# Kernel tuning notes

Hardware: AMD Instinct MI355X
Metric: run time of the kernel (lower is better)

Reference implementation:

```python
import jax, jax.numpy as jnp
import numpy as np

D = 8       # latent dim d
NE = 4      # n_emb
NS = 3      # n_outer stages
NI = 5      # n_inner iterations per stage
EPS = 1e-5  # LayerNorm eps
TAU = 1.0   # route_tau (default), max(1.0, 1e-3) = 1.0


def _ln(x, g, b):
    m = x.mean(-1, keepdims=True)
    v = ((x - m) ** 2).mean(-1, keepdims=True)
    return (x - m) / jnp.sqrt(v + EPS) * g + b


def _inner(E, u, Bm, Wp, bp, W1, b1, W2, b2):
    # E: [B, NE, D], u: [B, D]
    Bsz = E.shape[0]
    # bilinear interaction: outer product e_i u^T + B_i, for all i at once
    M = E[:, :, :, None] * u[:, None, None, :] + Bm[None]      # [B, NE, D, D]
    H = M.reshape(Bsz, NE, D * D) @ Wp.T + bp                  # W_proj: [B, NE, D]
    # softmax routing: s_i = softmax(route(h_i)/tau) over experts
    lg = jax.nn.relu(H @ W1.T + b1) @ W2.T + b2                # [B, NE, NE]
    s = jax.nn.softmax(lg / TAU, axis=-1)
    mix = jnp.einsum('bne,bed->bnd', s, H)                     # per-i mixture of H
    return E + mix


def setup_inputs() -> dict:
    B = 131072
    key = jax.random.key(0)
    ks = jax.random.split(key, 32)
    f32 = jnp.float32
    inp = {
        'cl':     jax.random.normal(ks[0], (B,), f32),
        'cd':     jax.random.normal(ks[1], (B,), f32),
        're_log': jax.random.normal(ks[2], (B,), f32),
        'mach':   jax.random.normal(ks[3], (B,), f32),
        'alpha':  jax.random.normal(ks[4], (B,), f32),
        'u':      jax.random.normal(ks[5], (B, D), f32),
        'We':    jax.random.normal(ks[6], (NE, D, 2), f32) * 0.5,
        'be':    jnp.zeros((NE, D), f32),
        # per-stage InnerBlockAblated params (stacked over NS stages)
        'Bmat':  jax.random.normal(ks[7], (NS, NE, D, D), f32) * 0.05,
        'Wproj': jax.random.normal(ks[8], (NS, D, D * D), f32) * 0.1,
        'bproj': jnp.zeros((NS, D), f32),
        'Wr1':   jax.random.normal(ks[9], (NS, D, D), f32) * 0.3,
        'br1':   jnp.zeros((NS, D), f32),
        'Wr2':   jax.random.normal(ks[10], (NS, NE, D), f32) * 0.3,
        'br2':   jnp.zeros((NS, NE), f32),
        # post-stage LayerNorm
        'ln_g':  jnp.ones((D,), f32),
        'ln_b':  jnp.zeros((D,), f32),
        # final mixing over embeddings: Linear(n_emb*d, n_emb)
        'Wout':  jax.random.normal(ks[11], (NE, NE * D), f32) * 0.1,
        'bout':  jnp.zeros((NE,), f32),
        # final LayerNorm
        'fg':    jnp.ones((D,), f32),
        'fb':    jnp.zeros((D,), f32),
        # heads: head_cst Linear(d, 18), head_cl Linear(d, 1)
        'Wcst':  jax.random.normal(ks[12], (18, D), f32) * 0.2,
        'bcst':  jnp.zeros((18,), f32),
        'Wcl':   jax.random.normal(ks[13], (1, D), f32) * 0.2,
        'bcl':   jnp.zeros((1,), f32),
    }
    return inp


def reference(cl, cd, re_log, mach, alpha, u, We, be, Bmat, Wproj, bproj,
              Wr1, br1, Wr2, br2, ln_g, ln_b, Wout, bout, fg, fb,
              Wcst, bcst, Wcl, bcl):
    # _stack_pairs: [B, 4, 2]
    pairs = jnp.stack([
        jnp.stack([cl, alpha], -1),
        jnp.stack([cd, alpha], -1),
        jnp.stack([re_log, alpha], -1),
        jnp.stack([mach, alpha], -1),
    ], axis=1)
    # embed: per-embedding Linear(2, d) + Tanh  -> E: [B, NE, D]
    E = jnp.tanh(jnp.einsum('bne,nde->bnd', pairs, We) + be[None])
    # outer stages: n_inner inner blocks each, then post-stage LayerNorm
    for s_idx in range(NS):
        for _ in range(NI):
            E = _inner(E, u, Bmat[s_idx], Wproj[s_idx], bproj[s_idx],
                       Wr1[s_idx], br1[s_idx], Wr2[s_idx], br2[s_idx])
        E = _ln(E, ln_g, ln_b)
    # final softmax mixing over embeddings (w_out_logits)
    Bsz = E.shape[0]
    w = jax.nn.softmax(E.reshape(Bsz, NE * D) @ Wout.T + bout, axis=-1)  # [B, NE]
    z = _ln(jnp.einsum('bn,bnd->bd', w, E), fg, fb)                       # [B, D]
    # heads, concatenated: [B, 18 + 1]
    return jnp.concatenate([z @ Wcst.T + bcst, z @ Wcl.T + bcl], axis=-1)
```

## Files before the change

kernel.cpp:

```cpp
#include <hip/hip_runtime.h>

#define D 8
#define NE 4
#define NS 3
#define NI 5
#define LN_EPS 1e-5f

#define OFF_W1 0
#define OFF_W2 192
#define OFF_B1 288
#define OFF_B2 312
#define OFF_C  324
#define OFF_LN 420
#define OFF_WP 436
#define WLDS_SIZE 1972

__global__ void precompute_C_kernel(const float* __restrict__ Bmat,
                                    const float* __restrict__ Wproj,
                                    const float* __restrict__ bproj,
                                    float* __restrict__ C) {
    int idx = threadIdx.x;
    if (idx >= NS * NE * D) return;
    int s = idx / (NE * D);
    int rem = idx % (NE * D);
    int n = rem / D;
    int d = rem % D;
    const float* bm = Bmat + ((size_t)s * NE + n) * 64;
    const float* wp = Wproj + ((size_t)s * D + d) * 64;
    float acc = bproj[s * D + d];
    #pragma unroll
    for (int k = 0; k < 64; ++k) acc += bm[k] * wp[k];
    C[idx] = acc;
}

__device__ __forceinline__ float fast_tanh(float x) {
    float e = __expf(2.f * x);
    return 1.f - 2.f * __builtin_amdgcn_rcpf(e + 1.f);
}

__device__ __forceinline__ float4 ld4(const float* p) {
    return *reinterpret_cast<const float4*>(p);
}

__global__ __launch_bounds__(256, 2) void whisp_kernel(
    const float* __restrict__ cl, const float* __restrict__ cd,
    const float* __restrict__ re_log, const float* __restrict__ mach,
    const float* __restrict__ alpha, const float* __restrict__ u,
    const float* __restrict__ We, const float* __restrict__ be,
    const float* __restrict__ Wproj,
    const float* __restrict__ Wr1, const float* __restrict__ br1,
    const float* __restrict__ Wr2, const float* __restrict__ br2,
    const float* __restrict__ ln_g, const float* __restrict__ ln_b,
    const float* __restrict__ Wout, const float* __restrict__ bout,
    const float* __restrict__ fg, const float* __restrict__ fb,
    const float* __restrict__ Wcst, const float* __restrict__ bcst,
    const float* __restrict__ Wcl, const float* __restrict__ bcl,
    const float* __restrict__ Cpre,
    float* __restrict__ out, int B)
{
    __shared__ __align__(16) float wlds[WLDS_SIZE];
    __shared__ __align__(16) float4 tbuf[16 * 256];

    const int tid = threadIdx.x;
    const int row0 = blockIdx.x * 256 + tid;
    const bool active = (row0 < B);
    const int row = active ? row0 : (B - 1);

    for (int i = tid; i < 192;  i += 256) wlds[OFF_W1 + i] = Wr1[i];
    for (int i = tid; i < 96;   i += 256) wlds[OFF_W2 + i] = Wr2[i];
    for (int i = tid; i < 24;   i += 256) wlds[OFF_B1 + i] = br1[i];
    for (int i = tid; i < 12;   i += 256) wlds[OFF_B2 + i] = br2[i];
    for (int i = tid; i < 96;   i += 256) wlds[OFF_C + i]  = Cpre[i];
    for (int i = tid; i < 8;    i += 256) { wlds[OFF_LN + i] = ln_g[i]; wlds[OFF_LN + 8 + i] = ln_b[i]; }
    for (int i = tid; i < 1536; i += 256) wlds[OFF_WP + i] = Wproj[i];

    float uu[D];
    {
        const float4* up = reinterpret_cast<const float4*>(u + (size_t)row * D);
        float4 u0 = up[0], u1 = up[1];
        uu[0]=u0.x; uu[1]=u0.y; uu[2]=u0.z; uu[3]=u0.w;
        uu[4]=u1.x; uu[5]=u1.y; uu[6]=u1.z; uu[7]=u1.w;
    }
    float xs[NE] = { cl[row], cd[row], re_log[row], mach[row] };
    float al = alpha[row];

    float E[NE][D];
    #pragma unroll
    for (int n = 0; n < NE; ++n) {
        #pragma unroll
        for (int d = 0; d < D; ++d) {
            float pre = We[n * 16 + d * 2 + 0] * xs[n]
                      + We[n * 16 + d * 2 + 1] * al
                      + be[n * D + d];
            E[n][d] = fast_tanh(pre);
        }
    }

    __syncthreads();

    int zero = 0;

    #pragma unroll 1
    for (int s = 0; s < NS; ++s) {
        {
            const float* Wp = wlds + OFF_WP + s * 512;
            #pragma unroll
            for (int d = 0; d < D; ++d) {
                float tv[D];
                #pragma unroll
                for (int i = 0; i < D; ++i) {
                    float4 wa = ld4(Wp + d * 64 + i * 8);
                    float4 wb = ld4(Wp + d * 64 + i * 8 + 4);
                    float a0 = uu[0] * wa.x, a1 = uu[1] * wa.y;
                    a0 = fmaf(uu[2], wa.z, a0); a1 = fmaf(uu[3], wa.w, a1);
                    a0 = fmaf(uu[4], wb.x, a0); a1 = fmaf(uu[5], wb.y, a1);
                    a0 = fmaf(uu[6], wb.z, a0); a1 = fmaf(uu[7], wb.w, a1);
                    tv[i] = a0 + a1;
                }
                tbuf[(2 * d) * 256 + tid]     = make_float4(tv[0], tv[1], tv[2], tv[3]);
                tbuf[(2 * d + 1) * 256 + tid] = make_float4(tv[4], tv[5], tv[6], tv[7]);
            }
        }

        float b1a[8], b2a[4];
        {
            float4 q0 = ld4(wlds + OFF_B1 + s * 8);
            float4 q1 = ld4(wlds + OFF_B1 + s * 8 + 4);
            b1a[0]=q0.x; b1a[1]=q0.y; b1a[2]=q0.z; b1a[3]=q0.w;
            b1a[4]=q1.x; b1a[5]=q1.y; b1a[6]=q1.z; b1a[7]=q1.w;
            float4 q2 = ld4(wlds + OFF_B2 + s * 4);
            b2a[0]=q2.x; b2a[1]=q2.y; b2a[2]=q2.z; b2a[3]=q2.w;
        }

        #pragma unroll 1
        for (int it = 0; it < NI; ++it) {
            asm volatile("" : "+v"(zero));
            const float*  W1z = wlds + OFF_W1 + s * 64 + zero;
            const float*  W2z = wlds + OFF_W2 + s * 32 + zero;
            const float*  Cz  = wlds + OFF_C  + s * 32 + zero;
            const float4* tz  = tbuf + tid + zero;

            float H[NE][D];
            #pragma unroll
            for (int n = 0; n < NE; ++n) {
                float4 c0 = ld4(Cz + n * 8);
                float4 c1 = ld4(Cz + n * 8 + 4);
                H[n][0]=c0.x; H[n][1]=c0.y; H[n][2]=c0.z; H[n][3]=c0.w;
                H[n][4]=c1.x; H[n][5]=c1.y; H[n][6]=c1.z; H[n][7]=c1.w;
            }
            #pragma unroll
            for (int d = 0; d < D; ++d) {
                float4 ta = tz[(2 * d) * 256];
                float4 tb = tz[(2 * d + 1) * 256];
                #pragma unroll
                for (int n = 0; n < NE; ++n) {
                    float a0 = fmaf(E[n][0], ta.x, H[n][d]);
                    float a1 = E[n][1] * ta.y;
                    a0 = fmaf(E[n][2], ta.z, a0);
                    a1 = fmaf(E[n][3], ta.w, a1);
                    a0 = fmaf(E[n][4], tb.x, a0);
                    a1 = fmaf(E[n][5], tb.y, a1);
                    a0 = fmaf(E[n][6], tb.z, a0);
                    a1 = fmaf(E[n][7], tb.w, a1);
                    H[n][d] = a0 + a1;
                }
            }

            float sm[NE][NE];
            #pragma unroll
            for (int n = 0; n < NE; ++n) {
                float r[D];
                #pragma unroll
                for (int d = 0; d < D; ++d) {
                    float4 wa = ld4(W1z + d * 8);
                    float4 wb = ld4(W1z + d * 8 + 4);
                    float a0 = fmaf(H[n][0], wa.x, b1a[d]);
                    float a1 = H[n][1] * wa.y;
                    a0 = fmaf(H[n][2], wa.z, a0);
                    a1 = fmaf(H[n][3], wa.w, a1);
                    a0 = fmaf(H[n][4], wb.x, a0);
                    a1 = fmaf(H[n][5], wb.y, a1);
                    a0 = fmaf(H[n][6], wb.z, a0);
                    a1 = fmaf(H[n][7], wb.w, a1);
                    r[d] = fmaxf(a0 + a1, 0.f);
                }
                float lg[NE];
                #pragma unroll
                for (int e = 0; e < NE; ++e) {
                    float4 wa = ld4(W2z + e * 8);
                    float4 wb = ld4(W2z + e * 8 + 4);
                    float a0 = fmaf(r[0], wa.x, b2a[e]);
                    float a1 = r[1] * wa.y;
                    a0 = fmaf(r[2], wa.z, a0);
                    a1 = fmaf(r[3], wa.w, a1);
                    a0 = fmaf(r[4], wb.x, a0);
                    a1 = fmaf(r[5], wb.y, a1);
                    a0 = fmaf(r[6], wb.z, a0);
                    a1 = fmaf(r[7], wb.w, a1);
                    lg[e] = a0 + a1;
                }
                float mx = fmaxf(fmaxf(lg[0], lg[1]), fmaxf(lg[2], lg[3]));
                float e0 = __expf(lg[0] - mx), e1 = __expf(lg[1] - mx);
                float e2 = __expf(lg[2] - mx), e3 = __expf(lg[3] - mx);
                float inv = __builtin_amdgcn_rcpf((e0 + e1) + (e2 + e3));
                sm[n][0] = e0 * inv; sm[n][1] = e1 * inv;
                sm[n][2] = e2 * inv; sm[n][3] = e3 * inv;
            }

            #pragma unroll
            for (int n = 0; n < NE; ++n) {
                #pragma unroll
                for (int d = 0; d < D; ++d) {
                    float a0 = fmaf(sm[n][0], H[0][d], E[n][d]);
                    float a1 = sm[n][1] * H[1][d];
                    a0 = fmaf(sm[n][2], H[2][d], a0);
                    a1 = fmaf(sm[n][3], H[3][d], a1);
                    E[n][d] = a0 + a1;
                }
            }
        }

        float lngv[8], lnbv[8];
        {
            float4 g0 = ld4(wlds + OFF_LN),     g1 = ld4(wlds + OFF_LN + 4);
            float4 b0 = ld4(wlds + OFF_LN + 8), b1 = ld4(wlds + OFF_LN + 12);
            lngv[0]=g0.x; lngv[1]=g0.y; lngv[2]=g0.z; lngv[3]=g0.w;
            lngv[4]=g1.x; lngv[5]=g1.y; lngv[6]=g1.z; lngv[7]=g1.w;
            lnbv[0]=b0.x; lnbv[1]=b0.y; lnbv[2]=b0.z; lnbv[3]=b0.w;
            lnbv[4]=b1.x; lnbv[5]=b1.y; lnbv[6]=b1.z; lnbv[7]=b1.w;
        }
        #pragma unroll
        for (int n = 0; n < NE; ++n) {
            float m = 0.f;
            #pragma unroll
            for (int d = 0; d < D; ++d) m += E[n][d];
            m *= (1.f / D);
            float v = 0.f;
            #pragma unroll
            for (int d = 0; d < D; ++d) { float c = E[n][d] - m; v = fmaf(c, c, v); }
            v *= (1.f / D);
            float inv = __builtin_amdgcn_rsqf(v + LN_EPS);
            #pragma unroll
            for (int d = 0; d < D; ++d)
                E[n][d] = (E[n][d] - m) * inv * lngv[d] + lnbv[d];
        }
    }

    float lgf[NE];
    #pragma unroll
    for (int e = 0; e < NE; ++e) {
        float a0 = bout[e], a1 = 0.f;
        #pragma unroll
        for (int n = 0; n < NE; ++n) {
            #pragma unroll
            for (int d = 0; d < D; d += 2) {
                a0 = fmaf(E[n][d],     Wout[e * 32 + n * D + d],     a0);
                a1 = fmaf(E[n][d + 1], Wout[e * 32 + n * D + d + 1], a1);
            }
        }
        lgf[e] = a0 + a1;
    }
    float mx = fmaxf(fmaxf(lgf[0], lgf[1]), fmaxf(lgf[2], lgf[3]));
    float w0 = __expf(lgf[0] - mx), w1 = __expf(lgf[1] - mx);
    float w2 = __expf(lgf[2] - mx), w3 = __expf(lgf[3] - mx);
    float winv = __builtin_amdgcn_rcpf((w0 + w1) + (w2 + w3));
    w0 *= winv; w1 *= winv; w2 *= winv; w3 *= winv;

    float z[D];
    #pragma unroll
    for (int d = 0; d < D; ++d) {
        float a0 = w0 * E[0][d];
        float a1 = w1 * E[1][d];
        a0 = fmaf(w2, E[2][d], a0);
        a1 = fmaf(w3, E[3][d], a1);
        z[d] = a0 + a1;
    }
    float zm = 0.f;
    #pragma unroll
    for (int d = 0; d < D; ++d) zm += z[d];
    zm *= (1.f / D);
    float zv = 0.f;
    #pragma unroll
    for (int d = 0; d < D; ++d) { float c = z[d] - zm; zv = fmaf(c, c, zv); }
    zv *= (1.f / D);
    float zinv = __builtin_amdgcn_rsqf(zv + LN_EPS);
    #pragma unroll
    for (int d = 0; d < D; ++d)
        z[d] = (z[d] - zm) * zinv * fg[d] + fb[d];

    float zout[19];
    #pragma unroll
    for (int k = 0; k < 18; ++k) {
        float a0 = bcst[k], a1 = 0.f;
        #pragma unroll
        for (int d = 0; d < D; d += 2) {
            a0 = fmaf(z[d],     Wcst[k * D + d],     a0);
            a1 = fmaf(z[d + 1], Wcst[k * D + d + 1], a1);
        }
        zout[k] = a0 + a1;
    }
    {
        float a0 = bcl[0], a1 = 0.f;
        #pragma unroll
        for (int d = 0; d < D; d += 2) {
            a0 = fmaf(z[d],     Wcl[d],     a0);
            a1 = fmaf(z[d + 1], Wcl[d + 1], a1);
        }
        zout[18] = a0 + a1;
    }

    __syncthreads();
    float* souts = reinterpret_cast<float*>(tbuf);
    if (active) {
        #pragma unroll
        for (int k = 0; k < 19; ++k) souts[tid * 19 + k] = zout[k];
    }
    __syncthreads();

    const int base = blockIdx.x * 256;
    int nrows = B - base;
    if (nrows > 256) nrows = 256;
    if (nrows > 0) {
        const int cnt = nrows * 19;
        for (int i = tid; i < cnt; i += 256)
            out[(size_t)base * 19 + i] = souts[i];
    }
}

extern "C" void kernel_launch(void* const* d_in, const int* in_sizes, int n_in,
                              void* d_out, int out_size, void* d_ws, size_t ws_size,
                              hipStream_t stream) {
    const float* cl     = (const float*)d_in[0];
    const float* cd     = (const float*)d_in[1];
    const float* re_log = (const float*)d_in[2];
    const float* mach   = (const float*)d_in[3];
    const float* alpha  = (const float*)d_in[4];
    const float* u      = (const float*)d_in[5];
    const float* We     = (const float*)d_in[6];
    const float* be     = (const float*)d_in[7];
    const float* Bmat   = (const float*)d_in[8];
    const float* Wproj  = (const float*)d_in[9];
    const float* bproj  = (const float*)d_in[10];
    const float* Wr1    = (const float*)d_in[11];
    const float* br1    = (const float*)d_in[12];
    const float* Wr2    = (const float*)d_in[13];
    const float* br2    = (const float*)d_in[14];
    const float* ln_g   = (const float*)d_in[15];
    const float* ln_b   = (const float*)d_in[16];
    const float* Wout   = (const float*)d_in[17];
    const float* bout   = (const float*)d_in[18];
    const float* fg     = (const float*)d_in[19];
    const float* fb     = (const float*)d_in[20];
    const float* Wcst   = (const float*)d_in[21];
    const float* bcst   = (const float*)d_in[22];
    const float* Wcl    = (const float*)d_in[23];
    const float* bcl    = (const float*)d_in[24];

    float* Cpre = (float*)d_ws;
    const int B = in_sizes[0];

    hipLaunchKernelGGL(precompute_C_kernel, dim3(1), dim3(128), 0, stream,
                       Bmat, Wproj, bproj, Cpre);

    const int blocks = (B + 255) / 256;
    hipLaunchKernelGGL(whisp_kernel, dim3(blocks), dim3(256), 0, stream,
                       cl, cd, re_log, mach, alpha, u, We, be, Wproj,
                       Wr1, br1, Wr2, br2, ln_g, ln_b, Wout, bout, fg, fb,
                       Wcst, bcst, Wcl, bcl, Cpre, (float*)d_out, B);
}
```

Baseline: 72.29 us.

## Vectorize inner block with packed float2 FMAs across embedding pairs

Reorganizes the per-row state so pairs of embeddings are held in float2 vectors, letting the compiler emit packed FP32 FMA instructions (v_pk_fma_f32) for the bilinear projection, routing MLP, softmax mixing and LayerNorm. The C precompute and W2 weights are relaid out in shared memory to match the paired layout, and the router's two layers are fused so logits accumulate directly per hidden unit. This aims to halve VALU instruction count in the compute-bound inner loop, at the cost of broadcast operand shuffles and possible register pressure changes.

```diff
diff --git a/kernel.cpp b/kernel.cpp
--- a/kernel.cpp
+++ b/kernel.cpp
@@ -6,14 +6,20 @@
 #define NI 5
 #define LN_EPS 1e-5f
 
-#define OFF_W1 0
-#define OFF_W2 192
-#define OFF_B1 288
-#define OFF_B2 312
-#define OFF_C  324
-#define OFF_LN 420
-#define OFF_WP 436
+#define OFF_W1  0
+#define OFF_W2T 192
+#define OFF_B1  288
+#define OFF_B2  312
+#define OFF_C   324
+#define OFF_LN  420
+#define OFF_WP  436
 #define WLDS_SIZE 1972
+
+typedef float f2 __attribute__((ext_vector_type(2)));
+
+__device__ __forceinline__ f2 fma2(f2 a, f2 b, f2 c) { return __builtin_elementwise_fma(a, b, c); }
+__device__ __forceinline__ f2 max2(f2 a, f2 b) { return __builtin_elementwise_max(a, b); }
+__device__ __forceinline__ f2 bc(float s) { return (f2){s, s}; }
 
 __global__ void precompute_C_kernel(const float* __restrict__ Bmat,
                                     const float* __restrict__ Wproj,
@@ -30,7 +36,7 @@
     float acc = bproj[s * D + d];
     #pragma unroll
     for (int k = 0; k < 64; ++k) acc += bm[k] * wp[k];
-    C[idx] = acc;
+    C[s * 32 + ((n >> 1) * 8 + d) * 2 + (n & 1)] = acc;
 }
 
 __device__ __forceinline__ float fast_tanh(float x) {
@@ -67,7 +73,10 @@
     const int row = active ? row0 : (B - 1);
 
     for (int i = tid; i < 192;  i += 256) wlds[OFF_W1 + i] = Wr1[i];
-    for (int i = tid; i < 96;   i += 256) wlds[OFF_W2 + i] = Wr2[i];
+    for (int i = tid; i < 96;   i += 256) {
+        int s = i / 32, rem = i % 32, d = rem / 4, e = rem % 4;
+        wlds[OFF_W2T + i] = Wr2[s * 32 + e * 8 + d];
+    }
     for (int i = tid; i < 24;   i += 256) wlds[OFF_B1 + i] = br1[i];
     for (int i = tid; i < 12;   i += 256) wlds[OFF_B2 + i] = br2[i];
     for (int i = tid; i < 96;   i += 256) wlds[OFF_C + i]  = Cpre[i];
@@ -84,15 +93,15 @@
     float xs[NE] = { cl[row], cd[row], re_log[row], mach[row] };
     float al = alpha[row];
 
-    float E[NE][D];
-    #pragma unroll
-    for (int n = 0; n < NE; ++n) {
+    f2 E2[2][D];
+    #pragma unroll
+    for (int nn = 0; nn < 2; ++nn) {
         #pragma unroll
         for (int d = 0; d < D; ++d) {
-            float pre = We[n * 16 + d * 2 + 0] * xs[n]
-                      + We[n * 16 + d * 2 + 1] * al
-                      + be[n * D + d];
-            E[n][d] = fast_tanh(pre);
+            int na = 2 * nn, nb = 2 * nn + 1;
+            float pa = We[na * 16 + d * 2] * xs[na] + We[na * 16 + d * 2 + 1] * al + be[na * D + d];
+            float pb = We[nb * 16 + d * 2] * xs[nb] + We[nb * 16 + d * 2 + 1] * al + be[nb * D + d];
+            E2[nn][d] = (f2){ fast_tanh(pa), fast_tanh(pb) };
         }
     }
 
@@ -104,6 +113,7 @@
     for (int s = 0; s < NS; ++s) {
         {
             const float* Wp = wlds + OFF_WP + s * 512;
+            f2 uu2[4] = { {uu[0],uu[1]}, {uu[2],uu[3]}, {uu[4],uu[5]}, {uu[6],uu[7]} };
             #pragma unroll
             for (int d = 0; d < D; ++d) {
                 float tv[D];
@@ -111,11 +121,11 @@
                 for (int i = 0; i < D; ++i) {
                     float4 wa = ld4(Wp + d * 64 + i * 8);
                     float4 wb = ld4(Wp + d * 64 + i * 8 + 4);
-                    float a0 = uu[0] * wa.x, a1 = uu[1] * wa.y;
-                    a0 = fmaf(uu[2], wa.z, a0); a1 = fmaf(uu[3], wa.w, a1);
-                    a0 = fmaf(uu[4], wb.x, a0); a1 = fmaf(uu[5], wb.y, a1);
-                    a0 = fmaf(uu[6], wb.z, a0); a1 = fmaf(uu[7], wb.w, a1);
-                    tv[i] = a0 + a1;
+                    f2 acc = uu2[0] * (f2){wa.x, wa.y};
+                    acc = fma2(uu2[1], (f2){wa.z, wa.w}, acc);
+                    acc = fma2(uu2[2], (f2){wb.x, wb.y}, acc);
+                    acc = fma2(uu2[3], (f2){wb.z, wb.w}, acc);
+                    tv[i] = acc.x + acc.y;
                 }
                 tbuf[(2 * d) * 256 + tid]     = make_float4(tv[0], tv[1], tv[2], tv[3]);
                 tbuf[(2 * d + 1) * 256 + tid] = make_float4(tv[4], tv[5], tv[6], tv[7]);
@@ -135,87 +145,96 @@
         #pragma unroll 1
         for (int it = 0; it < NI; ++it) {
             asm volatile("" : "+v"(zero));
-            const float*  W1z = wlds + OFF_W1 + s * 64 + zero;
-            const float*  W2z = wlds + OFF_W2 + s * 32 + zero;
-            const float*  Cz  = wlds + OFF_C  + s * 32 + zero;
-            const float4* tz  = tbuf + tid + zero;
-
-            float H[NE][D];
-            #pragma unroll
-            for (int n = 0; n < NE; ++n) {
-                float4 c0 = ld4(Cz + n * 8);
-                float4 c1 = ld4(Cz + n * 8 + 4);
-                H[n][0]=c0.x; H[n][1]=c0.y; H[n][2]=c0.z; H[n][3]=c0.w;
-                H[n][4]=c1.x; H[n][5]=c1.y; H[n][6]=c1.z; H[n][7]=c1.w;
+            const float*  W1z  = wlds + OFF_W1  + s * 64 + zero;
+            const float*  W2Tz = wlds + OFF_W2T + s * 32 + zero;
+            const float*  Cz   = wlds + OFF_C   + s * 32 + zero;
+            const float4* tz   = tbuf + tid + zero;
+
+            f2 H2[2][D];
+            #pragma unroll
+            for (int nn = 0; nn < 2; ++nn) {
+                #pragma unroll
+                for (int dp = 0; dp < 4; ++dp) {
+                    float4 cq = ld4(Cz + nn * 16 + dp * 4);
+                    H2[nn][2 * dp]     = (f2){cq.x, cq.y};
+                    H2[nn][2 * dp + 1] = (f2){cq.z, cq.w};
+                }
             }
             #pragma unroll
             for (int d = 0; d < D; ++d) {
                 float4 ta = tz[(2 * d) * 256];
                 float4 tb = tz[(2 * d + 1) * 256];
                 #pragma unroll
-                for (int n = 0; n < NE; ++n) {
-                    float a0 = fmaf(E[n][0], ta.x, H[n][d]);
-                    float a1 = E[n][1] * ta.y;
-                    a0 = fmaf(E[n][2], ta.z, a0);
-                    a1 = fmaf(E[n][3], ta.w, a1);
-                    a0 = fmaf(E[n][4], tb.x, a0);
-                    a1 = fmaf(E[n][5], tb.y, a1);
-                    a0 = fmaf(E[n][6], tb.z, a0);
-                    a1 = fmaf(E[n][7], tb.w, a1);
-                    H[n][d] = a0 + a1;
-                }
-            }
-
-            float sm[NE][NE];
-            #pragma unroll
-            for (int n = 0; n < NE; ++n) {
-                float r[D];
-                #pragma unroll
-                for (int d = 0; d < D; ++d) {
-                    float4 wa = ld4(W1z + d * 8);
-                    float4 wb = ld4(W1z + d * 8 + 4);
-                    float a0 = fmaf(H[n][0], wa.x, b1a[d]);
-                    float a1 = H[n][1] * wa.y;
-                    a0 = fmaf(H[n][2], wa.z, a0);
-                    a1 = fmaf(H[n][3], wa.w, a1);
-                    a0 = fmaf(H[n][4], wb.x, a0);
-                    a1 = fmaf(H[n][5], wb.y, a1);
-                    a0 = fmaf(H[n][6], wb.z, a0);
-                    a1 = fmaf(H[n][7], wb.w, a1);
-                    r[d] = fmaxf(a0 + a1, 0.f);
-                }
-                float lg[NE];
+                for (int nn = 0; nn < 2; ++nn) {
+                    f2 acc = H2[nn][d];
+                    acc = fma2(E2[nn][0], bc(ta.x), acc);
+                    acc = fma2(E2[nn][1], bc(ta.y), acc);
+                    acc = fma2(E2[nn][2], bc(ta.z), acc);
+                    acc = fma2(E2[nn][3], bc(ta.w), acc);
+                    acc = fma2(E2[nn][4], bc(tb.x), acc);
+                    acc = fma2(E2[nn][5], bc(tb.y), acc);
+                    acc = fma2(E2[nn][6], bc(tb.z), acc);
+                    acc = fma2(E2[nn][7], bc(tb.w), acc);
+                    H2[nn][d] = acc;
+                }
+            }
+
+            f2 lg2[2][NE];
+            #pragma unroll
+            for (int nn = 0; nn < 2; ++nn)
+                #pragma unroll
+                for (int e = 0; e < NE; ++e) lg2[nn][e] = bc(b2a[e]);
+
+            #pragma unroll
+            for (int d = 0; d < D; ++d) {
+                float4 wa = ld4(W1z + d * 8);
+                float4 wb = ld4(W1z + d * 8 + 4);
+                float4 w2 = ld4(W2Tz + d * 4);
+                #pragma unroll
+                for (int nn = 0; nn < 2; ++nn) {
+                    f2 acc = bc(b1a[d]);
+                    acc = fma2(H2[nn][0], bc(wa.x), acc);
+                    acc = fma2(H2[nn][1], bc(wa.y), acc);
+                    acc = fma2(H2[nn][2], bc(wa.z), acc);
+                    acc = fma2(H2[nn][3], bc(wa.w), acc);
+                    acc = fma2(H2[nn][4], bc(wb.x), acc);
+                    acc = fma2(H2[nn][5], bc(wb.y), acc);
+                    acc = fma2(H2[nn][6], bc(wb.z), acc);
+                    acc = fma2(H2[nn][7], bc(wb.w), acc);
+                    f2 r2 = max2(acc, bc(0.f));
+                    lg2[nn][0] = fma2(r2, bc(w2.x), lg2[nn][0]);
+                    lg2[nn][1] = fma2(r2, bc(w2.y), lg2[nn][1]);
+                    lg2[nn][2] = fma2(r2, bc(w2.z), lg2[nn][2]);
+                    lg2[nn][3] = fma2(r2, bc(w2.w), lg2[nn][3]);
+                }
+            }
+
+            f2 sm2[2][NE];
+            #pragma unroll
+            for (int nn = 0; nn < 2; ++nn) {
+                f2 m2 = max2(max2(lg2[nn][0], lg2[nn][1]), max2(lg2[nn][2], lg2[nn][3]));
+                f2 ee[NE];
                 #pragma unroll
                 for (int e = 0; e < NE; ++e) {
-                    float4 wa = ld4(W2z + e * 8);
-                    float4 wb = ld4(W2z + e * 8 + 4);
-                    float a0 = fmaf(r[0], wa.x, b2a[e]);
-                    float a1 = r[1] * wa.y;
-                    a0 = fmaf(r[2], wa.z, a0);
-                    a1 = fmaf(r[3], wa.w, a1);
-                    a0 = fmaf(r[4], wb.x, a0);
-                    a1 = fmaf(r[5], wb.y, a1);
-                    a0 = fmaf(r[6], wb.z, a0);
-                    a1 = fmaf(r[7], wb.w, a1);
-                    lg[e] = a0 + a1;
-                }
-                float mx = fmaxf(fmaxf(lg[0], lg[1]), fmaxf(lg[2], lg[3]));
-                float e0 = __expf(lg[0] - mx), e1 = __expf(lg[1] - mx);
-                float e2 = __expf(lg[2] - mx), e3 = __expf(lg[3] - mx);
-                float inv = __builtin_amdgcn_rcpf((e0 + e1) + (e2 + e3));
-                sm[n][0] = e0 * inv; sm[n][1] = e1 * inv;
-                sm[n][2] = e2 * inv; sm[n][3] = e3 * inv;
-            }
-
-            #pragma unroll
-            for (int n = 0; n < NE; ++n) {
-                #pragma unroll
-                for (int d = 0; d < D; ++d) {
-                    float a0 = fmaf(sm[n][0], H[0][d], E[n][d]);
-                    float a1 = sm[n][1] * H[1][d];
-                    a0 = fmaf(sm[n][2], H[2][d], a0);
-                    a1 = fmaf(sm[n][3], H[3][d], a1);
-                    E[n][d] = a0 + a1;
+                    f2 t = lg2[nn][e] - m2;
+                    ee[e] = (f2){ __expf(t.x), __expf(t.y) };
+                }
+                f2 s2 = (ee[0] + ee[1]) + (ee[2] + ee[3]);
+                f2 inv2 = (f2){ __builtin_amdgcn_rcpf(s2.x), __builtin_amdgcn_rcpf(s2.y) };
+                #pragma unroll
+                for (int e = 0; e < NE; ++e) sm2[nn][e] = ee[e] * inv2;
+            }
+
+            #pragma unroll
+            for (int d = 0; d < D; ++d) {
+                #pragma unroll
+                for (int nn = 0; nn < 2; ++nn) {
+                    f2 acc = E2[nn][d];
+                    acc = fma2(sm2[nn][0], bc(H2[0][d].x), acc);
+                    acc = fma2(sm2[nn][1], bc(H2[0][d].y), acc);
+                    acc = fma2(sm2[nn][2], bc(H2[1][d].x), acc);
+                    acc = fma2(sm2[nn][3], bc(H2[1][d].y), acc);
+                    E2[nn][d] = acc;
                 }
             }
         }
@@ -230,19 +249,19 @@
             lnbv[4]=b1.x; lnbv[5]=b1.y; lnbv[6]=b1.z; lnbv[7]=b1.w;
         }
         #pragma unroll
-        for (int n = 0; n < NE; ++n) {
-            float m = 0.f;
-            #pragma unroll
-            for (int d = 0; d < D; ++d) m += E[n][d];
-            m *= (1.f / D);
-            float v = 0.f;
-            #pragma unroll
-            for (int d = 0; d < D; ++d) { float c = E[n][d] - m; v = fmaf(c, c, v); }
-            v *= (1.f / D);
-            float inv = __builtin_amdgcn_rsqf(v + LN_EPS);
+        for (int nn = 0; nn < 2; ++nn) {
+            f2 s2 = (E2[nn][0] + E2[nn][1]) + (E2[nn][2] + E2[nn][3]);
+            s2 = s2 + (E2[nn][4] + E2[nn][5]) + (E2[nn][6] + E2[nn][7]);
+            f2 m2 = s2 * bc(0.125f);
+            f2 v2 = bc(0.f);
+            #pragma unroll
+            for (int d = 0; d < D; ++d) { f2 c = E2[nn][d] - m2; v2 = fma2(c, c, v2); }
+            v2 = v2 * bc(0.125f);
+            f2 inv2 = (f2){ __builtin_amdgcn_rsqf(v2.x + LN_EPS),
+                            __builtin_amdgcn_rsqf(v2.y + LN_EPS) };
             #pragma unroll
             for (int d = 0; d < D; ++d)
-                E[n][d] = (E[n][d] - m) * inv * lngv[d] + lnbv[d];
+                E2[nn][d] = fma2((E2[nn][d] - m2) * inv2, bc(lngv[d]), bc(lnbv[d]));
         }
     }
 
@@ -251,12 +270,11 @@
     for (int e = 0; e < NE; ++e) {
         float a0 = bout[e], a1 = 0.f;
         #pragma unroll
-        for (int n = 0; n < NE; ++n) {
-            #pragma unroll
-            for (int d = 0; d < D; d += 2) {
-                a0 = fmaf(E[n][d],     Wout[e * 32 + n * D + d],     a0);
-                a1 = fmaf(E[n][d + 1], Wout[e * 32 + n * D + d + 1], a1);
-            }
+        for (int d = 0; d < D; ++d) {
+            a0 = fmaf(E2[0][d].x, Wout[e * 32 + 0 * D + d], a0);
+            a1 = fmaf(E2[0][d].y, Wout[e * 32 + 1 * D + d], a1);
+            a0 = fmaf(E2[1][d].x, Wout[e * 32 + 2 * D + d], a0);
+            a1 = fmaf(E2[1][d].y, Wout[e * 32 + 3 * D + d], a1);
         }
         lgf[e] = a0 + a1;
     }
@@ -269,10 +287,10 @@
     float z[D];
     #pragma unroll
     for (int d = 0; d < D; ++d) {
-        float a0 = w0 * E[0][d];
-        float a1 = w1 * E[1][d];
-        a0 = fmaf(w2, E[2][d], a0);
-        a1 = fmaf(w3, E[3][d], a1);
+        float a0 = w0 * E2[0][d].x;
+        float a1 = w1 * E2[0][d].y;
+        a0 = fmaf(w2, E2[1][d].x, a0);
+        a1 = fmaf(w3, E2[1][d].y, a1);
         z[d] = a0 + a1;
     }
     float zm = 0.f;
```

New measurement: 65.21 us. 9.8% less time.
